# Optimization experiments

Measured on AMD Instinct MI355X. Metric: run time of the kernel, lower is better.

The kernel has to match this reference:

```python
import jax, jax.numpy as jnp
import numpy as np

CHEB_K = 3
HIDDEN = 64
HORIZON = 12
OUT_DIM = 1


def _supports(E, K):
    # adaptive adjacency: softmax(relu(E E^T)) rows, Chebyshev polynomial stack [K, N, N]
    A = jax.nn.softmax(jax.nn.relu(E @ E.T), axis=1)
    N = E.shape[0]
    s = [jnp.eye(N, dtype=E.dtype), A]
    for _ in range(2, K):
        s.append(2.0 * (A @ s[-1]) - s[-2])
    return jnp.stack(s, axis=0)


def _gconv(x, supports, W, b):
    # x: [B,N,C], supports: [K,N,N], W: [N,K,C,O], b: [N,O] -> [B,N,O]
    xg = jnp.einsum('knm,bmc->bnkc', supports, x)
    return jnp.einsum('bnkc,nkco->bno', xg, W) + b


def _agcrn_layer(x_seq, supports, gW, gb, uW, ub):
    # x_seq: [B,T,N,C]; returns full hidden sequence [B,T,N,H]
    B, T, N, _ = x_seq.shape
    h0 = jnp.zeros((B, N, HIDDEN), dtype=x_seq.dtype)

    def step(h, x):
        zr = jax.nn.sigmoid(_gconv(jnp.concatenate([x, h], axis=-1), supports, gW, gb))
        z, r = zr[..., :HIDDEN], zr[..., HIDDEN:]
        hc = jnp.tanh(_gconv(jnp.concatenate([x, z * h], axis=-1), supports, uW, ub))
        h_new = r * h + (1.0 - r) * hc
        return h_new, h_new

    _, hs = jax.lax.scan(step, h0, jnp.swapaxes(x_seq, 0, 1))  # [T,B,N,H]
    return jnp.swapaxes(hs, 0, 1)


def _forward(source, E, pools, conv_w, conv_b):
    supports = _supports(E, CHEB_K)
    cur = source
    for (gwp, gbp, uwp, ubp) in pools:
        # per-node weights from embedding pool (hoisted: E is constant over time)
        gW = jnp.einsum('nd,dkio->nkio', E, gwp)
        gb = E @ gbp
        uW = jnp.einsum('nd,dkio->nkio', E, uwp)
        ub = E @ ubp
        cur = _agcrn_layer(cur, supports, gW, gb, uW, ub)
    last = cur[:, -1]  # [B,N,H]
    # end_conv: Conv2d(1, horizon*out_dim, kernel=(1,H)) == linear over H per node
    y = jnp.einsum('bnh,oh->bon', last, conv_w) + conv_b[None, :, None]  # [B, horizon*out, N]
    B, _, N = y.shape
    y = y.reshape(B, HORIZON, OUT_DIM, N).transpose(0, 1, 3, 2)  # [B, horizon, N, out_dim]
    return y


def setup_inputs() -> dict:
    key = jax.random.key(0)
    ks = jax.random.split(key, 12)
    B, T, N, C, D, H = 64, 12, 2000, 1, 16, HIDDEN
    s = 0.1  # keep gates/tanh unsaturated
    return {
        'source': jax.random.normal(ks[0], (B, T, N, C), jnp.float32),
        'node_embeddings': jax.random.normal(ks[1], (N, D), jnp.float32),
        'gate_wpool_0': jax.random.normal(ks[2], (D, CHEB_K, C + H, 2 * H), jnp.float32) * s,
        'gate_bpool_0': jax.random.normal(ks[3], (D, 2 * H), jnp.float32) * s,
        'update_wpool_0': jax.random.normal(ks[4], (D, CHEB_K, C + H, H), jnp.float32) * s,
        'update_bpool_0': jax.random.normal(ks[5], (D, H), jnp.float32) * s,
        'gate_wpool_1': jax.random.normal(ks[6], (D, CHEB_K, 2 * H, 2 * H), jnp.float32) * s,
        'gate_bpool_1': jax.random.normal(ks[7], (D, 2 * H), jnp.float32) * s,
        'update_wpool_1': jax.random.normal(ks[8], (D, CHEB_K, 2 * H, H), jnp.float32) * s,
        'update_bpool_1': jax.random.normal(ks[9], (D, H), jnp.float32) * s,
        'conv_w': jax.random.normal(ks[10], (HORIZON * OUT_DIM, H), jnp.float32) * s,
        'conv_b': jax.random.normal(ks[11], (HORIZON * OUT_DIM,), jnp.float32) * s,
    }


def reference(source, node_embeddings, gate_wpool_0, gate_bpool_0, update_wpool_0,
              update_bpool_0, gate_wpool_1, gate_bpool_1, update_wpool_1,
              update_bpool_1, conv_w, conv_b):
    pools = [
        (gate_wpool_0, gate_bpool_0, update_wpool_0, update_bpool_0),
        (gate_wpool_1, gate_bpool_1, update_wpool_1, update_bpool_1),
    ]
    return _forward(source, node_embeddings, pools, conv_w, conv_b)
```

## Files before the change

kernel.cpp:

```cpp
#include <hip/hip_runtime.h>
#include <hip/hip_bf16.h>
#include <math.h>

#define NN 2000
#define DD 16
#define BB 64
#define TT 12
#define HH 64
#define MR 4000
#define SCL 2048.0f
#define ISCL (1.0f / 2048.0f)

typedef _Float16 f16;
typedef __attribute__((ext_vector_type(8))) _Float16 frag8h;
typedef __attribute__((ext_vector_type(4))) float floatx4;

__device__ inline float fin(float v) {
  return (v == v && v > -1e30f && v < 1e30f) ? v : 0.f;
}
__device__ inline float sigmoid_safe(float x) {
  float e = expf(-fabsf(x));
  float s = 1.f / (1.f + e);
  return x >= 0.f ? s : 1.f - s;
}
__device__ inline float tanh_safe(float x) {
  float e = expf(-2.f * fabsf(x));
  float r = (1.f - e) / (1.f + e);
  return x >= 0.f ? r : -r;
}
__device__ inline void split16(float v, f16& hi, f16& lo) {
  hi = (f16)v;
  lo = (f16)((v - (float)hi) * SCL);
}
__device__ inline void gll16(const void* g, void* l) {
  __builtin_amdgcn_global_load_lds((const __attribute__((address_space(1))) void*)g,
                                   (__attribute__((address_space(3))) void*)l, 16, 0, 0);
}

__global__ void kzero(float* p, int n) {
  int i = blockIdx.x * 256 + threadIdx.x;
  if (i < n) p[i] = 0.f;
}

__global__ __launch_bounds__(256) void ka(const float* __restrict__ E,
                                          float* __restrict__ A) {
  __shared__ float s[NN];
  __shared__ float red[256];
  int n = blockIdx.x;
  float en[DD];
#pragma unroll
  for (int d = 0; d < DD; ++d) en[d] = fin(E[n * DD + d]);
  float lmax = 0.f;
  for (int m = threadIdx.x; m < NN; m += 256) {
    float acc = 0.f;
#pragma unroll
    for (int d = 0; d < DD; ++d) acc += en[d] * fin(E[m * DD + d]);
    acc = fmaxf(acc, 0.f);
    s[m] = acc;
    lmax = fmaxf(lmax, acc);
  }
  red[threadIdx.x] = lmax;
  __syncthreads();
  for (int w = 128; w > 0; w >>= 1) {
    if (threadIdx.x < w) red[threadIdx.x] = fmaxf(red[threadIdx.x], red[threadIdx.x + w]);
    __syncthreads();
  }
  float mx = red[0];
  __syncthreads();
  float lsum = 0.f;
  for (int m = threadIdx.x; m < NN; m += 256) {
    float e = expf(s[m] - mx);
    s[m] = e;
    lsum += e;
  }
  red[threadIdx.x] = lsum;
  __syncthreads();
  for (int w = 128; w > 0; w >>= 1) {
    if (threadIdx.x < w) red[threadIdx.x] += red[threadIdx.x + w];
    __syncthreads();
  }
  float inv = 1.f / red[0];
  for (int m = threadIdx.x; m < NN; m += 256) A[(size_t)n * NN + m] = s[m] * inv;
}

#define TM 64
#define TK 32
__global__ __launch_bounds__(256) void kg(const float* __restrict__ A,
                                          const float* __restrict__ V,
                                          float* __restrict__ C, int cols) {
  __shared__ float As[TK][TM + 1];
  __shared__ float Bs[TK][TM + 1];
  int r0 = blockIdx.x * TM;
  int c0 = blockIdx.y * TM;
  int tid = threadIdx.x;
  int tx = tid % 16;
  int ty = tid / 16;
  float acc[4][4];
#pragma unroll
  for (int i = 0; i < 4; ++i)
#pragma unroll
    for (int j = 0; j < 4; ++j) acc[i][j] = 0.f;
  for (int k0 = 0; k0 < NN; k0 += TK) {
    for (int i = tid; i < TM * TK; i += 256) {
      int rr = i / TK, kk = i % TK;
      int gr = r0 + rr, gk = k0 + kk;
      As[kk][rr] = (gr < NN && gk < NN) ? A[(size_t)gr * NN + gk] : 0.f;
    }
    for (int i = tid; i < TK * TM; i += 256) {
      int kk = i / TM, cc = i % TM;
      int gk = k0 + kk, gc = c0 + cc;
      Bs[kk][cc] = (gk < NN && gc < cols) ? V[(size_t)gk * cols + gc] : 0.f;
    }
    __syncthreads();
#pragma unroll 4
    for (int kk = 0; kk < TK; ++kk) {
      float a[4], b[4];
#pragma unroll
      for (int i = 0; i < 4; ++i) a[i] = As[kk][ty * 4 + i];
#pragma unroll
      for (int j = 0; j < 4; ++j) b[j] = Bs[kk][tx * 4 + j];
#pragma unroll
      for (int i = 0; i < 4; ++i)
#pragma unroll
        for (int j = 0; j < 4; ++j) acc[i][j] += a[i] * b[j];
    }
    __syncthreads();
  }
#pragma unroll
  for (int i = 0; i < 4; ++i) {
    int gr = r0 + ty * 4 + i;
    if (gr >= NN) continue;
#pragma unroll
    for (int j = 0; j < 4; ++j) {
      int gc = c0 + tx * 4 + j;
      if (gc < cols) C[(size_t)gr * cols + gc] = acc[i][j];
    }
  }
}

__global__ void ksplitM(const float* __restrict__ A, const float* __restrict__ A2,
                        f16* __restrict__ Mh, f16* __restrict__ Ml) {
  int i = blockIdx.x * 256 + threadIdx.x;
  if (i >= MR * NN) return;
  int m = i / NN;
  int k = i % NN;
  float v;
  if (m < NN) v = A[(size_t)m * NN + k];
  else {
    int mm = m - NN;
    v = 2.f * A2[(size_t)mm * NN + k] - (mm == k ? 1.f : 0.f);
  }
  f16 hi, lo;
  split16(v, hi, lo);
  Mh[i] = hi;
  Ml[i] = lo;
}

__global__ __launch_bounds__(256) void kconvT(const float* __restrict__ V,
                                              f16* __restrict__ Th,
                                              f16* __restrict__ Tl, int cols) {
  __shared__ float sh[32][33];
  int k0 = blockIdx.x * 32;
  int c0 = blockIdx.y * 32;
  int tx = threadIdx.x % 32;
  int ty = threadIdx.x / 32;
#pragma unroll
  for (int i = 0; i < 4; ++i) {
    int r = k0 + ty + i * 8;
    int c = c0 + tx;
    sh[ty + i * 8][tx] = (r < NN && c < cols) ? V[(size_t)r * cols + c] : 0.f;
  }
  __syncthreads();
#pragma unroll
  for (int i = 0; i < 4; ++i) {
    int cc = c0 + ty + i * 8;
    int kk = k0 + tx;
    if (cc < cols && kk < NN) {
      f16 hi, lo;
      split16(sh[tx][ty + i * 8], hi, lo);
      Th[(size_t)cc * NN + kk] = hi;
      Tl[(size_t)cc * NN + kk] = lo;
    }
  }
}

#define KT 32
__global__ __launch_bounds__(256, 2) void kmm(const f16* __restrict__ Mh,
                                              const f16* __restrict__ Ml,
                                              const f16* __restrict__ Bh,
                                              const f16* __restrict__ Bl,
                                              float* __restrict__ C1,
                                              float* __restrict__ C2, int cols) {
  __shared__ __align__(16) f16 Ash[2][128 * KT];
  __shared__ __align__(16) f16 Asl[2][128 * KT];
  __shared__ __align__(16) f16 Bsh[2][128 * KT];
  __shared__ __align__(16) f16 Bsl[2][128 * KT];
  int tid = threadIdx.x;
  int lane = tid & 63;
  int wave = tid >> 6;
  int wr = wave >> 1;
  int wc = wave & 1;
  int gx = gridDim.x;
  int nwg = gx * gridDim.y;
  int wg = blockIdx.y * gx + blockIdx.x;
  int q = nwg >> 3, r = nwg & 7;
  int xcd = wg & 7, lid = wg >> 3;
  int swz = (xcd < r ? xcd * (q + 1) : r * (q + 1) + (xcd - r) * q) + lid;
  int bx = swz % gx;
  int by = swz / gx;
  floatx4 acc0[4][4], acc1[4][4];
#pragma unroll
  for (int i = 0; i < 4; ++i)
#pragma unroll
    for (int j = 0; j < 4; ++j) {
      acc0[i][j] = (floatx4){0.f, 0.f, 0.f, 0.f};
      acc1[i][j] = (floatx4){0.f, 0.f, 0.f, 0.f};
    }
  const frag8h zf = {0, 0, 0, 0, 0, 0, 0, 0};

  auto comp = [&](int buf) {
    frag8h ah[4], al[4], bh[4], bl[4];
#pragma unroll
    for (int mi = 0; mi < 4; ++mi) {
      int jr = wr * 4 + mi;
      ah[mi] = *(const frag8h*)(&Ash[buf][jr * 512 + lane * 8]);
      al[mi] = *(const frag8h*)(&Asl[buf][jr * 512 + lane * 8]);
    }
#pragma unroll
    for (int ni = 0; ni < 4; ++ni) {
      int jc = wc * 4 + ni;
      bh[ni] = *(const frag8h*)(&Bsh[buf][jc * 512 + lane * 8]);
      bl[ni] = *(const frag8h*)(&Bsl[buf][jc * 512 + lane * 8]);
    }
#pragma unroll
    for (int mi = 0; mi < 4; ++mi)
#pragma unroll
      for (int ni = 0; ni < 4; ++ni) {
        acc0[mi][ni] = __builtin_amdgcn_mfma_f32_16x16x32_f16(ah[mi], bh[ni], acc0[mi][ni], 0, 0, 0);
        acc1[mi][ni] = __builtin_amdgcn_mfma_f32_16x16x32_f16(ah[mi], bl[ni], acc1[mi][ni], 0, 0, 0);
        acc1[mi][ni] = __builtin_amdgcn_mfma_f32_16x16x32_f16(al[mi], bh[ni], acc1[mi][ni], 0, 0, 0);
      }
  };

  const int lr = lane & 15;
  const int lq = lane >> 4;
  auto stage = [&](int buf, int k0) {
#pragma unroll
    for (int jj = 0; jj < 2; ++jj) {
      int j = wave * 2 + jj;
      int r2 = j * 16 + lr;
      size_t ko = (size_t)k0 + lq * 8;
      int gra = bx * 128 + r2;
      if (gra >= MR) gra = MR - 1;
      gll16(Mh + (size_t)gra * NN + ko, &Ash[buf][j * 512]);
      gll16(Ml + (size_t)gra * NN + ko, &Asl[buf][j * 512]);
      int grb = by * 128 + r2;
      if (grb >= cols) grb = cols - 1;
      gll16(Bh + (size_t)grb * NN + ko, &Bsh[buf][j * 512]);
      gll16(Bl + (size_t)grb * NN + ko, &Bsl[buf][j * 512]);
    }
  };

  const int NK = NN / KT;
  stage(0, 0);
  int cur = 0;
  for (int ks = 0; ks < NK; ++ks) {
    if (ks + 1 < NK) {
      stage(cur ^ 1, (ks + 1) * KT);
      asm volatile("s_waitcnt vmcnt(8)" ::: "memory");
    } else {
      asm volatile("s_waitcnt vmcnt(0)" ::: "memory");
    }
    __builtin_amdgcn_s_barrier();
    asm volatile("" ::: "memory");
    __builtin_amdgcn_sched_barrier(0);
    comp(cur);
    __builtin_amdgcn_sched_barrier(0);
    asm volatile("" ::: "memory");
    __builtin_amdgcn_s_barrier();
    cur ^= 1;
  }
  {
    int k0 = NK * KT;
    if (k0 < NN) {
      for (int c = tid; c < 512; c += 256) {
        int j = c >> 6;
        int ll = c & 63;
        int qq = ll >> 4;
        int rr = ll & 15;
        int r2 = j * 16 + rr;
        int gk = k0 + qq * 8;
        bool kok = (gk + 8 <= NN);
        int gra = bx * 128 + r2;
        bool aok = kok && (gra < MR);
        size_t ga = (size_t)gra * NN + gk;
        *(frag8h*)(&Ash[cur][c * 8]) = aok ? *(const frag8h*)(Mh + ga) : zf;
        *(frag8h*)(&Asl[cur][c * 8]) = aok ? *(const frag8h*)(Ml + ga) : zf;
        int grb = by * 128 + r2;
        bool bok = kok && (grb < cols);
        size_t gb = (size_t)grb * NN + gk;
        *(frag8h*)(&Bsh[cur][c * 8]) = bok ? *(const frag8h*)(Bh + gb) : zf;
        *(frag8h*)(&Bsl[cur][c * 8]) = bok ? *(const frag8h*)(Bl + gb) : zf;
      }
      __syncthreads();
      comp(cur);
      __syncthreads();
    }
  }
#pragma unroll
  for (int mi = 0; mi < 4; ++mi) {
#pragma unroll
    for (int ni = 0; ni < 4; ++ni) {
#pragma unroll
      for (int reg = 0; reg < 4; ++reg) {
        int row = bx * 128 + wr * 64 + mi * 16 + (lane >> 4) * 4 + reg;
        int col = by * 128 + wc * 64 + ni * 16 + (lane & 15);
        if (col >= cols || row >= MR) continue;
        float v = acc0[mi][ni][reg] + acc1[mi][ni][reg] * ISCL;
        if (row < NN) C1[(size_t)row * cols + col] = v;
        else C2[(size_t)(row - NN) * cols + col] = v;
      }
    }
  }
}

__global__ void kx(const float* __restrict__ src, float* __restrict__ xb,
                   int t, int b0, int CB) {
  int i = blockIdx.x * 256 + threadIdx.x;
  if (i >= NN * CB) return;
  int bb = i % CB;
  int n = i / CB;
  xb[i] = fin(src[((size_t)(b0 + bb) * TT + t) * NN + n]);
}

__global__ void kxa(const float* __restrict__ src, float* __restrict__ xa,
                    int b0, int CB) {
  int i = blockIdx.x * 256 + threadIdx.x;
  if (i >= NN * TT * CB) return;
  int bb = i % CB;
  int t = (i / CB) % TT;
  int n = i / (CB * TT);
  xa[i] = fin(src[((size_t)(b0 + bb) * TT + t) * NN + n]);
}

__global__ void kmulz(float* __restrict__ zb, const float* __restrict__ h, int n) {
  int i = blockIdx.x * 256 + threadIdx.x;
  if (i < n) zb[i] = zb[i] * h[i];
}

template <int O, int CB>
__global__ __launch_bounds__(256) void kgc(
    const float* __restrict__ x0, const float* __restrict__ x1, const float* __restrict__ x2,
    const float* __restrict__ wp, int Ctot, int base_c, int nC, int ldn,
    const float* __restrict__ E, const float* __restrict__ bp,
    int act, int accum, float* outA, float* outB,
    int update, const float* __restrict__ rb, float* hio) {
  __shared__ float xs[8][CB + 1];
  __shared__ float ws[8][O];
  __shared__ float esm[DD];
  int n = blockIdx.x;
  int tid = threadIdx.x;
  int to = tid % 16;
  int tb = tid / 16;
  if (tid < DD) esm[tid] = fin(E[n * DD + tid]);
  __syncthreads();
  constexpr int NO = O / 16;
  constexpr int NB = CB / 16;
  float acc[NB][NO];
#pragma unroll
  for (int i = 0; i < NB; ++i)
#pragma unroll
    for (int j = 0; j < NO; ++j) acc[i][j] = 0.f;
  const size_t nb = (size_t)n * CB;
  const size_t nx = (size_t)n * ldn;
  for (int k = 0; k < 3; ++k) {
    const float* xk = (k == 0) ? x0 : (k == 1) ? x1 : x2;
    for (int c0 = 0; c0 < nC; c0 += 8) {
      int chunk = (nC - c0 < 8) ? (nC - c0) : 8;
      for (int i = tid; i < chunk * CB; i += 256) {
        int cc = i % chunk;
        int b = i / chunk;
        xs[cc][b] = xk[nx + (size_t)b * nC + c0 + cc];
      }
      for (int i = tid; i < chunk * O; i += 256) {
        int o = i % O;
        int cc = i / O;
        int crow = base_c + c0 + cc;
        float wa = 0.f;
#pragma unroll
        for (int d = 0; d < DD; ++d)
          wa += esm[d] * fin(wp[((size_t)(d * 3 + k) * Ctot + crow) * O + o]);
        ws[cc][o] = wa;
      }
      __syncthreads();
      for (int cc = 0; cc < chunk; ++cc) {
        float xv[NB];
#pragma unroll
        for (int i = 0; i < NB; ++i) xv[i] = xs[cc][tb + 16 * i];
#pragma unroll
        for (int j = 0; j < NO; ++j) {
          float wv = ws[cc][to + 16 * j];
#pragma unroll
          for (int i = 0; i < NB; ++i) acc[i][j] += xv[i] * wv;
        }
      }
      __syncthreads();
    }
  }
#pragma unroll
  for (int i2 = 0; i2 < NB; ++i2) {
    int b = tb + 16 * i2;
#pragma unroll
    for (int j = 0; j < NO; ++j) {
      int o = to + 16 * j;
      float r = acc[i2][j];
      float* dst = (o < HH || !outB) ? (outA + (nb + b) * HH + (o % HH))
                                     : (outB + (nb + b) * HH + (o - HH));
      if (accum) r += *dst;
      if (bp) {
        float ba = 0.f;
#pragma unroll
        for (int d = 0; d < DD; ++d) ba += esm[d] * fin(bp[d * O + o]);
        r += ba;
      }
      r = fin(r);
      if (act == 1) r = sigmoid_safe(r);
      else if (act == 2) r = tanh_safe(r);
      if (update) {
        float rg = rb[(nb + b) * HH + o];
        float hold = hio[(nb + b) * HH + o];
        hio[(nb + b) * HH + o] = rg * hold + (1.f - rg) * r;
      } else {
        *dst = r;
      }
    }
  }
}

__global__ void kfin(const float* __restrict__ h1, const float* __restrict__ cw,
                     const float* __restrict__ cb, float* __restrict__ out,
                     int b0, int CB) {
  int idx = blockIdx.x * 256 + threadIdx.x;
  if (idx >= CB * TT * NN) return;
  int n = idx % NN;
  int o = (idx / NN) % TT;
  int bb = idx / (NN * TT);
  const float* hp = h1 + ((size_t)n * CB + bb) * HH;
  float acc = fin(cb[o]);
#pragma unroll
  for (int hh = 0; hh < HH; ++hh) acc += hp[hh] * fin(cw[o * HH + hh]);
  out[((size_t)(b0 + bb) * TT + o) * NN + n] = fin(acc);
}

template <int CB>
static void run_chunks(const float* src, const float* E,
                       const float* gwp0, const float* gbp0,
                       const float* uwp0, const float* ubp0,
                       const float* gwp1, const float* gbp1,
                       const float* uwp1, const float* ubp1,
                       const float* cw, const float* cb,
                       float* out, f16* Mh, f16* Ml,
                       char* wsp, size_t off0, bool roomy, hipStream_t stream) {
  size_t off = off0;
  auto allocf = [&](size_t nelem) {
    float* p = (float*)(wsp + off);
    off += (nelem * 4 + 255) & ~(size_t)255;
    return p;
  };
  auto alloch = [&](size_t nelem) {
    f16* p = (f16*)(wsp + off);
    off += (nelem * 2 + 255) & ~(size_t)255;
    return p;
  };
  const int C = CB * HH;
  const int XC = TT * CB;
  const size_t NC = (size_t)NN * C;
  float* P1  = allocf(NC);
  float* P2  = allocf(NC);
  float* h0  = allocf(NC);
  float* h1  = allocf(NC);
  float* zb  = allocf(NC);
  float* rbf = allocf(NC);
  float* hc  = allocf(NC);
  f16* vh = alloch(NC);
  f16* vl = alloch(NC);
  float *P1c = nullptr, *P2c = nullptr;
  float *xa = nullptr, *xb1a = nullptr, *xb2a = nullptr;
  float *xb0 = nullptr, *xb1 = nullptr, *xb2 = nullptr;
  f16 *xth, *xtl;
  if (roomy) {
    P1c = allocf(NC);
    P2c = allocf(NC);
    xa   = allocf((size_t)NN * XC);
    xb1a = allocf((size_t)NN * XC);
    xb2a = allocf((size_t)NN * XC);
    xth = alloch((size_t)NN * XC);
    xtl = alloch((size_t)NN * XC);
  } else {
    xb0 = allocf((size_t)NN * CB);
    xb1 = allocf((size_t)NN * CB);
    xb2 = allocf((size_t)NN * CB);
    xth = alloch((size_t)NN * CB);
    xtl = alloch((size_t)NN * CB);
  }

  const int EW = (int)((NC + 255) / 256);
  const dim3 gConv((NN + 31) / 32, (C + 31) / 32);
  const dim3 gMM((MR + 127) / 128, (C + 127) / 128);
  float* nul = nullptr;

  auto chain_to = [&](const float* V, float* D1, float* D2) {
    kconvT<<<gConv, 256, 0, stream>>>(V, vh, vl, C);
    kmm<<<gMM, 256, 0, stream>>>(Mh, Ml, vh, vl, D1, D2, C);
  };

  for (int b0 = 0; b0 < BB; b0 += CB) {
    kzero<<<EW, 256, 0, stream>>>(h0, (int)NC);
    kzero<<<EW, 256, 0, stream>>>(h1, (int)NC);
    if (roomy) {
      kxa<<<((NN * XC) + 255) / 256, 256, 0, stream>>>(src, xa, b0, CB);
      dim3 gcx((NN + 31) / 32, (XC + 31) / 32);
      kconvT<<<gcx, 256, 0, stream>>>(xa, xth, xtl, XC);
      dim3 gmx((MR + 127) / 128, (XC + 127) / 128);
      kmm<<<gmx, 256, 0, stream>>>(Mh, Ml, xth, xtl, xb1a, xb2a, XC);
    }
    for (int t = 0; t < TT; ++t) {
      const bool tz = (t == 0);
      const float *xt0, *xt1, *xt2;
      int xln;
      if (roomy) {
        xt0 = xa + t * CB;
        xt1 = xb1a + t * CB;
        xt2 = xb2a + t * CB;
        xln = XC;
      } else {
        kx<<<(NN * CB + 255) / 256, 256, 0, stream>>>(src, xb0, t, b0, CB);
        dim3 gcx((NN + 31) / 32, (CB + 31) / 32);
        kconvT<<<gcx, 256, 0, stream>>>(xb0, xth, xtl, CB);
        dim3 gmx((MR + 127) / 128, (CB + 127) / 128);
        kmm<<<gmx, 256, 0, stream>>>(Mh, Ml, xth, xtl, xb1, xb2, CB);
        xt0 = xb0; xt1 = xb1; xt2 = xb2;
        xln = CB;
      }
      const float *g1, *g2;
      if (tz) { g1 = h0; g2 = h0; }
      else if (roomy) { g1 = P1c; g2 = P2c; }
      else { chain_to(h0, P1, P2); g1 = P1; g2 = P2; }
      kgc<128, CB><<<NN, 256, 0, stream>>>(h0, g1, g2, gwp0, 65, 1, 64, C, E, nullptr,
                                           0, 0, zb, rbf, 0, nul, nul);
      kgc<128, CB><<<NN, 256, 0, stream>>>(xt0, xt1, xt2, gwp0, 65, 0, 1, xln, E, gbp0,
                                           1, 1, zb, rbf, 0, nul, nul);
      kgc<64, CB><<<NN, 256, 0, stream>>>(xt0, xt1, xt2, uwp0, 65, 0, 1, xln, E, nullptr,
                                          0, 0, hc, nul, 0, nul, nul);
      kmulz<<<EW, 256, 0, stream>>>(zb, h0, (int)NC);
      if (tz) {
        kgc<64, CB><<<NN, 256, 0, stream>>>(zb, zb, zb, uwp0, 65, 1, 64, C, E, ubp0,
                                            2, 1, hc, nul, 1, rbf, h0);
      } else {
        chain_to(zb, P1, P2);
        kgc<64, CB><<<NN, 256, 0, stream>>>(zb, P1, P2, uwp0, 65, 1, 64, C, E, ubp0,
                                            2, 1, hc, nul, 1, rbf, h0);
      }
      if (tz) {
        kgc<128, CB><<<NN, 256, 0, stream>>>(h1, h1, h1, gwp1, 128, 64, 64, C, E, nullptr,
                                             0, 0, zb, rbf, 0, nul, nul);
      } else {
        chain_to(h1, P1, P2);
        kgc<128, CB><<<NN, 256, 0, stream>>>(h1, P1, P2, gwp1, 128, 64, 64, C, E, nullptr,
                                             0, 0, zb, rbf, 0, nul, nul);
      }
      float* q1 = roomy ? P1c : P1;
      float* q2 = roomy ? P2c : P2;
      chain_to(h0, q1, q2);
      kgc<128, CB><<<NN, 256, 0, stream>>>(h0, q1, q2, gwp1, 128, 0, 64, C, E, gbp1,
                                           1, 1, zb, rbf, 0, nul, nul);
      kgc<64, CB><<<NN, 256, 0, stream>>>(h0, q1, q2, uwp1, 128, 0, 64, C, E, nullptr,
                                          0, 0, hc, nul, 0, nul, nul);
      kmulz<<<EW, 256, 0, stream>>>(zb, h1, (int)NC);
      if (tz) {
        kgc<64, CB><<<NN, 256, 0, stream>>>(zb, zb, zb, uwp1, 128, 64, 64, C, E, ubp1,
                                            2, 1, hc, nul, 1, rbf, h1);
      } else {
        chain_to(zb, P1, P2);
        kgc<64, CB><<<NN, 256, 0, stream>>>(zb, P1, P2, uwp1, 128, 64, 64, C, E, ubp1,
                                            2, 1, hc, nul, 1, rbf, h1);
      }
    }
    kfin<<<(CB * TT * NN + 255) / 256, 256, 0, stream>>>(h1, cw, cb, out, b0, CB);
  }
}

extern "C" void kernel_launch(void* const* d_in, const int* in_sizes, int n_in,
                              void* d_out, int out_size, void* d_ws, size_t ws_size,
                              hipStream_t stream) {
  const float* src  = (const float*)d_in[0];
  const float* E    = (const float*)d_in[1];
  const float* gwp0 = (const float*)d_in[2];
  const float* gbp0 = (const float*)d_in[3];
  const float* uwp0 = (const float*)d_in[4];
  const float* ubp0 = (const float*)d_in[5];
  const float* gwp1 = (const float*)d_in[6];
  const float* gbp1 = (const float*)d_in[7];
  const float* uwp1 = (const float*)d_in[8];
  const float* ubp1 = (const float*)d_in[9];
  const float* cw   = (const float*)d_in[10];
  const float* cb   = (const float*)d_in[11];
  float* out = (float*)d_out;
  (void)in_sizes; (void)n_in; (void)out_size;

  char* wsp = (char*)d_ws;
  size_t off = 0;
  f16* Mh = (f16*)(wsp + off); off += ((size_t)MR * NN * 2 + 255) & ~(size_t)255;
  f16* Ml = (f16*)(wsp + off); off += ((size_t)MR * NN * 2 + 255) & ~(size_t)255;
  size_t off0 = off;
  float* A  = (float*)(wsp + off0);
  float* A2 = (float*)(wsp + off0 + (((size_t)NN * NN * 4 + 255) & ~(size_t)255));

  ka<<<NN, 256, 0, stream>>>(E, A);
  {
    dim3 g((NN + TM - 1) / TM, (NN + TM - 1) / TM);
    kg<<<g, 256, 0, stream>>>(A, A, A2, NN);
  }
  ksplitM<<<(MR * NN + 255) / 256, 256, 0, stream>>>(A, A2, Mh, Ml);

  if (ws_size >= (size_t)400 * 1000 * 1000) {
    run_chunks<64>(src, E, gwp0, gbp0, uwp0, ubp0, gwp1, gbp1, uwp1, ubp1,
                   cw, cb, out, Mh, Ml, wsp, off0, true, stream);
  } else if (ws_size >= (size_t)320 * 1000 * 1000) {
    run_chunks<64>(src, E, gwp0, gbp0, uwp0, ubp0, gwp1, gbp1, uwp1, ubp1,
                   cw, cb, out, Mh, Ml, wsp, off0, false, stream);
  } else if (ws_size >= (size_t)225 * 1000 * 1000) {
    run_chunks<32>(src, E, gwp0, gbp0, uwp0, ubp0, gwp1, gbp1, uwp1, ubp1,
                   cw, cb, out, Mh, Ml, wsp, off0, true, stream);
  } else if (ws_size >= (size_t)185 * 1000 * 1000) {
    run_chunks<32>(src, E, gwp0, gbp0, uwp0, ubp0, gwp1, gbp1, uwp1, ubp1,
                   cw, cb, out, Mh, Ml, wsp, off0, false, stream);
  } else if (ws_size >= (size_t)130 * 1000 * 1000) {
    run_chunks<16>(src, E, gwp0, gbp0, uwp0, ubp0, gwp1, gbp1, uwp1, ubp1,
                   cw, cb, out, Mh, Ml, wsp, off0, true, stream);
  } else {
    run_chunks<16>(src, E, gwp0, gbp0, uwp0, ubp0, gwp1, gbp1, uwp1, ubp1,
                   cw, cb, out, Mh, Ml, wsp, off0, false, stream);
  }
}
```

Before: 54.58 ms.

## Widen split-f16 MFMA GEMM tile to 128x256 with 8 waves per block

The kmm GEMM moves from 256-thread blocks computing 128x128 output tiles to 512-thread blocks computing 128x256 tiles. The B shared buffers double, and the staging loads are redistributed across 8 waves at 6 loads per wave, with the waitcnt adjusted to match. The goal is to reuse each staged A tile across twice as many columns, cutting global traffic for the large adjacency operand and halving the grid along the column dimension. In exchange, shared memory use rises to 96KB per block, which may limit occupancy. Fewer blocks could also underfill the GPU when the column count is small.

After: 73.75 ms. 1.35x slower.

```diff
diff --git a/kernel.cpp b/kernel.cpp
--- a/kernel.cpp
+++ b/kernel.cpp
@@ -185,7 +185,7 @@
 }
 
 #define KT 32
-__global__ __launch_bounds__(256, 2) void kmm(const f16* __restrict__ Mh,
+__global__ __launch_bounds__(512, 2) void kmm(const f16* __restrict__ Mh,
                                               const f16* __restrict__ Ml,
                                               const f16* __restrict__ Bh,
                                               const f16* __restrict__ Bl,
@@ -193,13 +193,13 @@
                                               float* __restrict__ C2, int cols) {
   __shared__ __align__(16) f16 Ash[2][128 * KT];
   __shared__ __align__(16) f16 Asl[2][128 * KT];
-  __shared__ __align__(16) f16 Bsh[2][128 * KT];
-  __shared__ __align__(16) f16 Bsl[2][128 * KT];
+  __shared__ __align__(16) f16 Bsh[2][256 * KT];
+  __shared__ __align__(16) f16 Bsl[2][256 * KT];
   int tid = threadIdx.x;
   int lane = tid & 63;
   int wave = tid >> 6;
-  int wr = wave >> 1;
-  int wc = wave & 1;
+  int wr = wave >> 2;
+  int wc = wave & 3;
   int gx = gridDim.x;
   int nwg = gx * gridDim.y;
   int wg = blockIdx.y * gx + blockIdx.x;
@@ -246,18 +246,26 @@
   const int lq = lane >> 4;
   auto stage = [&](int buf, int k0) {
 #pragma unroll
-    for (int jj = 0; jj < 2; ++jj) {
-      int j = wave * 2 + jj;
-      int r2 = j * 16 + lr;
+    for (int jj = 0; jj < 6; ++jj) {
+      int g = wave * 6 + jj;
       size_t ko = (size_t)k0 + lq * 8;
-      int gra = bx * 128 + r2;
-      if (gra >= MR) gra = MR - 1;
-      gll16(Mh + (size_t)gra * NN + ko, &Ash[buf][j * 512]);
-      gll16(Ml + (size_t)gra * NN + ko, &Asl[buf][j * 512]);
-      int grb = by * 128 + r2;
-      if (grb >= cols) grb = cols - 1;
-      gll16(Bh + (size_t)grb * NN + ko, &Bsh[buf][j * 512]);
-      gll16(Bl + (size_t)grb * NN + ko, &Bsl[buf][j * 512]);
+      if (g < 16) {
+        int j = g & 7;
+        int r2 = j * 16 + lr;
+        int gra = bx * 128 + r2;
+        if (gra >= MR) gra = MR - 1;
+        const f16* s = (g < 8) ? Mh : Ml;
+        f16* d = (g < 8) ? &Ash[buf][j * 512] : &Asl[buf][j * 512];
+        gll16(s + (size_t)gra * NN + ko, d);
+      } else {
+        int j = (g - 16) & 15;
+        int r2 = j * 16 + lr;
+        int grb = by * 256 + r2;
+        if (grb >= cols) grb = cols - 1;
+        const f16* s = (g < 32) ? Bh : Bl;
+        f16* d = (g < 32) ? &Bsh[buf][j * 512] : &Bsl[buf][j * 512];
+        gll16(s + (size_t)grb * NN + ko, d);
+      }
     }
   };
 
@@ -267,7 +275,7 @@
   for (int ks = 0; ks < NK; ++ks) {
     if (ks + 1 < NK) {
       stage(cur ^ 1, (ks + 1) * KT);
-      asm volatile("s_waitcnt vmcnt(8)" ::: "memory");
+      asm volatile("s_waitcnt vmcnt(6)" ::: "memory");
     } else {
       asm volatile("s_waitcnt vmcnt(0)" ::: "memory");
     }
@@ -283,24 +291,30 @@
   {
     int k0 = NK * KT;
     if (k0 < NN) {
-      for (int c = tid; c < 512; c += 256) {
-        int j = c >> 6;
+      for (int c = tid; c < 48 * 64; c += 512) {
+        int g = c >> 6;
         int ll = c & 63;
         int qq = ll >> 4;
         int rr = ll & 15;
-        int r2 = j * 16 + rr;
         int gk = k0 + qq * 8;
         bool kok = (gk + 8 <= NN);
-        int gra = bx * 128 + r2;
-        bool aok = kok && (gra < MR);
-        size_t ga = (size_t)gra * NN + gk;
-        *(frag8h*)(&Ash[cur][c * 8]) = aok ? *(const frag8h*)(Mh + ga) : zf;
-        *(frag8h*)(&Asl[cur][c * 8]) = aok ? *(const frag8h*)(Ml + ga) : zf;
-        int grb = by * 128 + r2;
-        bool bok = kok && (grb < cols);
-        size_t gb = (size_t)grb * NN + gk;
-        *(frag8h*)(&Bsh[cur][c * 8]) = bok ? *(const frag8h*)(Bh + gb) : zf;
-        *(frag8h*)(&Bsl[cur][c * 8]) = bok ? *(const frag8h*)(Bl + gb) : zf;
+        if (g < 16) {
+          int j = g & 7;
+          int gra = bx * 128 + j * 16 + rr;
+          bool aok = kok && (gra < MR);
+          size_t ga = (size_t)gra * NN + gk;
+          f16* d = (g < 8) ? &Ash[cur][j * 512 + ll * 8] : &Asl[cur][j * 512 + ll * 8];
+          const f16* s = (g < 8) ? Mh : Ml;
+          *(frag8h*)d = aok ? *(const frag8h*)(s + ga) : zf;
+        } else {
+          int j = (g - 16) & 15;
+          int grb = by * 256 + j * 16 + rr;
+          bool bok = kok && (grb < cols);
+          size_t gb = (size_t)grb * NN + gk;
+          f16* d = (g < 32) ? &Bsh[cur][j * 512 + ll * 8] : &Bsl[cur][j * 512 + ll * 8];
+          const f16* s = (g < 32) ? Bh : Bl;
+          *(frag8h*)d = bok ? *(const frag8h*)(s + gb) : zf;
+        }
       }
       __syncthreads();
       comp(cur);
@@ -314,7 +328,7 @@
 #pragma unroll
       for (int reg = 0; reg < 4; ++reg) {
         int row = bx * 128 + wr * 64 + mi * 16 + (lane >> 4) * 4 + reg;
-        int col = by * 128 + wc * 64 + ni * 16 + (lane & 15);
+        int col = by * 256 + wc * 64 + ni * 16 + (lane & 15);
         if (col >= cols || row >= MR) continue;
         float v = acc0[mi][ni][reg] + acc1[mi][ni][reg] * ISCL;
         if (row < NN) C1[(size_t)row * cols + col] = v;
@@ -506,12 +520,12 @@
 
   const int EW = (int)((NC + 255) / 256);
   const dim3 gConv((NN + 31) / 32, (C + 31) / 32);
-  const dim3 gMM((MR + 127) / 128, (C + 127) / 128);
+  const dim3 gMM((MR + 127) / 128, (C + 255) / 256);
   float* nul = nullptr;
 
   auto chain_to = [&](const float* V, float* D1, float* D2) {
     kconvT<<<gConv, 256, 0, stream>>>(V, vh, vl, C);
-    kmm<<<gMM, 256, 0, stream>>>(Mh, Ml, vh, vl, D1, D2, C);
+    kmm<<<gMM, 512, 0, stream>>>(Mh, Ml, vh, vl, D1, D2, C);
   };
 
   for (int b0 = 0; b0 < BB; b0 += CB) {
@@ -521,8 +535,8 @@
       kxa<<<((NN * XC) + 255) / 256, 256, 0, stream>>>(src, xa, b0, CB);
       dim3 gcx((NN + 31) / 32, (XC + 31) / 32);
       kconvT<<<gcx, 256, 0, stream>>>(xa, xth, xtl, XC);
-      dim3 gmx((MR + 127) / 128, (XC + 127) / 128);
-      kmm<<<gmx, 256, 0, stream>>>(Mh, Ml, xth, xtl, xb1a, xb2a, XC);
+      dim3 gmx((MR + 127) / 128, (XC + 255) / 256);
+      kmm<<<gmx, 512, 0, stream>>>(Mh, Ml, xth, xtl, xb1a, xb2a, XC);
     }
     for (int t = 0; t < TT; ++t) {
       const bool tz = (t == 0);
@@ -537,8 +551,8 @@
         kx<<<(NN * CB + 255) / 256, 256, 0, stream>>>(src, xb0, t, b0, CB);
         dim3 gcx((NN + 31) / 32, (CB + 31) / 32);
         kconvT<<<gcx, 256, 0, stream>>>(xb0, xth, xtl, CB);
-        dim3 gmx((MR + 127) / 128, (CB + 127) / 128);
-        kmm<<<gmx, 256, 0, stream>>>(Mh, Ml, xth, xtl, xb1, xb2, CB);
+        dim3 gmx((MR + 127) / 128, (CB + 255) / 256);
+        kmm<<<gmx, 512, 0, stream>>>(Mh, Ml, xth, xtl, xb1, xb2, CB);
         xt0 = xb0; xt1 = xb1; xt2 = xb2;
         xln = CB;
       }
```
